# Kernel tuning notes

Measured on AMD Instinct MI355X. Metric: run time of the kernel, lower is better.

Reference implementation:

```python
import jax, jax.numpy as jnp
import numpy as np

B, C, S_TGT, S_MEM, D, NH, DK, DHID = 8, 1, 2048, 1024, 512, 2, 64, 1024
DQ4 = float(DK) ** 0.25  # dim_q ** (1/4) scaling used by LightAttention


def _light_mask(S, E):
    # torch: log(triu(ones(E, S)).T) -> (S, E); 0 where col <= row else -inf
    return jnp.where(jnp.arange(E)[None, :] <= jnp.arange(S)[:, None], 0.0, -jnp.inf)


def _mhla(x_q, x_kv, Wq, bq, Wk, bk, Wv, bv, Wo, bo, use_mask):
    # Wq/Wk/Wv: (h, d_in, 64); per-head linear projections done batched via einsum
    Q = jnp.einsum('bcsd,hde->hbcse', x_q, Wq) + bq[:, None, None, None, :]
    K = jnp.einsum('bcsd,hde->hbcse', x_kv, Wk) + bk[:, None, None, None, :]
    V = jnp.einsum('bcsd,hde->hbcse', x_kv, Wv) + bv[:, None, None, None, :]
    if use_mask:
        Q = Q + _light_mask(Q.shape[-2], Q.shape[-1])
    A = jax.nn.softmax(Q / DQ4, axis=-2)                      # row-softmax over seq
    Kt = jnp.swapaxes(K, -1, -2) / DQ4                        # (h,b,c,64,Skv)
    Bm = jnp.einsum('hbces,hbcsd->hbced', jax.nn.softmax(Kt, axis=-1), V)  # (h,b,c,64,64)
    Z = jnp.einsum('hbcqe,hbced->hbcqd', A, Bm)               # (h,b,c,Sq,64)
    h, b, c, sq, dk = Z.shape
    Zc = jnp.moveaxis(Z, 0, -2).reshape(b, c, sq, h * dk)     # head-major concat
    return Zc @ Wo + bo


def _ln(x, g, bta, eps=1e-5):
    # torch LayerNorm over the last 3 dims (C,H,dim), biased variance
    mu = x.mean(axis=(-3, -2, -1), keepdims=True)
    var = ((x - mu) ** 2).mean(axis=(-3, -2, -1), keepdims=True)
    return (x - mu) / jnp.sqrt(var + eps) * g + bta


def _lffn(x, E1, D1, E2, D2):
    h = (x @ E1) @ D1           # dim -> dim_bn -> dim_hid
    h = h * jax.nn.sigmoid(h)   # Swish; dropout is identity in eval
    return (h @ E2) @ D2        # dim_hid -> dim_bn -> dim


def setup_inputs() -> dict:
    key = jax.random.key(0)
    ks = jax.random.split(key, 32)
    n = lambda i, shape, fan: jax.random.normal(ks[i], shape, jnp.float32) / np.sqrt(fan)
    inp = {
        'mem': jax.random.normal(ks[0], (B, C, S_MEM, D), jnp.float32),
        'y': jax.random.normal(ks[1], (B, C, S_TGT, D), jnp.float32),
        # masked self-attention MHLA (2 heads)
        'Wq_sa': n(2, (NH, D, DK), D), 'bq_sa': jnp.zeros((NH, DK), jnp.float32),
        'Wk_sa': n(3, (NH, D, DK), D), 'bk_sa': jnp.zeros((NH, DK), jnp.float32),
        'Wv_sa': n(4, (NH, D, DK), D), 'bv_sa': jnp.zeros((NH, DK), jnp.float32),
        'Wo_sa': n(5, (NH * DK, D), NH * DK), 'bo_sa': jnp.zeros((D,), jnp.float32),
        # cross-attention MHLA (2 heads)
        'Wq_x': n(6, (NH, D, DK), D), 'bq_x': jnp.zeros((NH, DK), jnp.float32),
        'Wk_x': n(7, (NH, D, DK), D), 'bk_x': jnp.zeros((NH, DK), jnp.float32),
        'Wv_x': n(8, (NH, D, DK), D), 'bv_x': jnp.zeros((NH, DK), jnp.float32),
        'Wo_x': n(9, (NH * DK, D), NH * DK), 'bo_x': jnp.zeros((D,), jnp.float32),
        # LFFN (bias-free linears); dim_bn = S_TGT
        'E1': n(10, (D, S_TGT), D), 'D1': n(11, (S_TGT, DHID), S_TGT),
        'E2': n(12, (DHID, S_TGT), DHID), 'D2': n(13, (S_TGT, D), S_TGT),
        # LayerNorm affines over (C, H, dim)
        'g1': jnp.ones((C, S_TGT, D), jnp.float32), 'b1': jnp.zeros((C, S_TGT, D), jnp.float32),
        'g2': jnp.ones((C, S_TGT, D), jnp.float32), 'b2': jnp.zeros((C, S_TGT, D), jnp.float32),
        'g3': jnp.ones((C, S_TGT, D), jnp.float32), 'b3': jnp.zeros((C, S_TGT, D), jnp.float32),
    }
    return inp


def reference(mem, y, Wq_sa, bq_sa, Wk_sa, bk_sa, Wv_sa, bv_sa, Wo_sa, bo_sa,
              Wq_x, bq_x, Wk_x, bk_x, Wv_x, bv_x, Wo_x, bo_x,
              E1, D1, E2, D2, g1, b1, g2, b2, g3, b3):
    y = y + _mhla(y, y, Wq_sa, bq_sa, Wk_sa, bk_sa, Wv_sa, bv_sa, Wo_sa, bo_sa, True)
    y = _ln(y, g1, b1)
    y = y + _mhla(y, mem, Wq_x, bq_x, Wk_x, bk_x, Wv_x, bv_x, Wo_x, bo_x, False)
    y = _ln(y, g2, b2)
    y = y + _lffn(y, E1, D1, E2, D2)
    y = _ln(y, g3, b3)
    return y
```

## Files before the change

### kernel.cpp

```cpp
#include <hip/hip_runtime.h>
#include <hip/hip_bf16.h>

#define BB 8
#define STGT 2048
#define SMEM 1024
#define DD 512
#define NHH 2
#define DKK 64
#define DHIDN 1024
#define NCH 32

static constexpr float INV_DQ4 = 0.35355339059327373f;

typedef __bf16 bf16x8 __attribute__((ext_vector_type(8)));
typedef float f32x4 __attribute__((ext_vector_type(4)));
typedef __hip_bfloat16 bf16_t;

__device__ __forceinline__ float ldext(const void* p, size_t i, int gbf) {
    return gbf ? __bfloat162float(((const bf16_t*)p)[i]) : ((const float*)p)[i];
}

__device__ __forceinline__ float4 ldext4(const void* p, size_t i, int gbf) {
    float4 v;
    if (gbf) {
        ushort4 u = *(const ushort4*)((const bf16_t*)p + i);
        v.x = __bfloat162float(*(const bf16_t*)&u.x);
        v.y = __bfloat162float(*(const bf16_t*)&u.y);
        v.z = __bfloat162float(*(const bf16_t*)&u.z);
        v.w = __bfloat162float(*(const bf16_t*)&u.w);
    } else {
        v = *(const float4*)((const float*)p + i);
    }
    return v;
}

__device__ __forceinline__ ushort4 packbf4(float4 v) {
    ushort4 o;
    bf16_t b0 = __float2bfloat16(v.x), b1 = __float2bfloat16(v.y);
    bf16_t b2 = __float2bfloat16(v.z), b3 = __float2bfloat16(v.w);
    o.x = *(unsigned short*)&b0;
    o.y = *(unsigned short*)&b1;
    o.z = *(unsigned short*)&b2;
    o.w = *(unsigned short*)&b3;
    return o;
}

__device__ __forceinline__ void gld16(const bf16_t* g, bf16_t* l) {
    __builtin_amdgcn_global_load_lds(
        (const __attribute__((address_space(1))) unsigned int*)g,
        (__attribute__((address_space(3))) unsigned int*)l, 16, 0, 0);
}

__device__ __forceinline__ void sm_combine_block(const float* __restrict__ pstat, int mat,
                                                 float* smx, float* sinv, int t) {
    if (t < 64) {
        const int col = t;
        float m = -1e30f;
#pragma unroll 4
        for (int c2 = 0; c2 < NCH; ++c2)
            m = fmaxf(m, pstat[(size_t)(mat * NCH + c2) * 128 + col]);
        float s = 0.f;
#pragma unroll 4
        for (int c2 = 0; c2 < NCH; ++c2) {
            float pm = pstat[(size_t)(mat * NCH + c2) * 128 + col];
            float ps = pstat[(size_t)(mat * NCH + c2) * 128 + 64 + col];
            s += ps * __expf(pm - m);
        }
        smx[col] = m;
        sinv[col] = 1.f / s;
    }
}

__global__ void detect_k(const unsigned int* __restrict__ g1w, int* __restrict__ flag,
                         float* __restrict__ statp) {
    for (int i = threadIdx.x; i < 12288; i += 256) statp[i] = 0.f;
    if (threadIdx.x == 0) flag[0] = (g1w[0] == 0x3F800000u) ? 0 : 1;
}

__global__ __launch_bounds__(256) void gemm64_k(
    const bf16_t* __restrict__ A, int lda,
    const bf16_t* __restrict__ Bt, int ldb,
    void* C, int ldc, int obf,
    const float* __restrict__ bias,
    const void* Res, int ldr, int resbf,
    int K, int act, float* __restrict__ lnstats)
{
    __shared__ __align__(16) char smem[32768];
    bf16_t* sA = (bf16_t*)smem;
    bf16_t* sB = (bf16_t*)(smem + 16384);
    float* T = (float*)smem;

    const int t = threadIdx.x, lane = t & 63, wave = t >> 6;

    int bx = blockIdx.x, by = blockIdx.y;
    const int nbx = gridDim.x, nby = gridDim.y;
    if ((nby & 7) == 0) {
        int ord = by * nbx + bx;
        int grp = ord / (nbx * 8);
        int rem = ord - grp * nbx * 8;
        by = grp * 8 + (rem & 7);
        bx = rem >> 3;
    }
    const int m0 = by * 64, n0 = bx * 64;

    const int srow = t >> 3;
    const int schunk = ((t & 7) ^ (srow & 7)) * 8;
    const bf16_t* Ag = A + (size_t)(m0 + srow) * lda + schunk;
    const bf16_t* Ag1 = Ag + (size_t)32 * lda;
    const bf16_t* Bg = Bt + (size_t)(n0 + srow) * ldb + schunk;
    const bf16_t* Bg1 = Bg + (size_t)32 * ldb;
    const int wofs = t * 8;

    const int wm = wave >> 1, wn = wave & 1;
    const int fr = lane & 15, quad = lane >> 4;
    const int f7 = fr & 7;

    f32x4 acc[2][2];
#pragma unroll
    for (int i = 0; i < 2; ++i)
#pragma unroll
        for (int j = 0; j < 2; ++j) acc[i][j] = (f32x4){0.f, 0.f, 0.f, 0.f};

    gld16(Ag, sA + wofs);
    gld16(Ag1, sA + wofs + 2048);
    gld16(Bg, sB + wofs);
    gld16(Bg1, sB + wofs + 2048);

    int cur = 0;
    for (int k0 = 0; k0 < K; k0 += 64) {
        __builtin_amdgcn_s_waitcnt(0x0070);
        __builtin_amdgcn_s_barrier();
        if (k0 + 64 < K) {
            const int nxt = cur ^ 1;
            gld16(Ag + k0 + 64, sA + nxt * 4096 + wofs);
            gld16(Ag1 + k0 + 64, sA + nxt * 4096 + wofs + 2048);
            gld16(Bg + k0 + 64, sB + nxt * 4096 + wofs);
            gld16(Bg1 + k0 + 64, sB + nxt * 4096 + wofs + 2048);
        }
        const bf16_t* ab = sA + cur * 4096;
        const bf16_t* bb = sB + cur * 4096;
        bf16x8 af[2][2], bfv[2][2];
#pragma unroll
        for (int mf = 0; mf < 2; ++mf)
#pragma unroll
            for (int ks = 0; ks < 2; ++ks)
                af[mf][ks] = *(const bf16x8*)(ab + (wm * 32 + mf * 16 + fr) * 64 +
                                              (((ks * 4 + quad) ^ f7) * 8));
#pragma unroll
        for (int nf = 0; nf < 2; ++nf)
#pragma unroll
            for (int ks = 0; ks < 2; ++ks)
                bfv[nf][ks] = *(const bf16x8*)(bb + (wn * 32 + nf * 16 + fr) * 64 +
                                               (((ks * 4 + quad) ^ f7) * 8));
#pragma unroll
        for (int ks = 0; ks < 2; ++ks)
#pragma unroll
            for (int mf = 0; mf < 2; ++mf)
#pragma unroll
                for (int nf = 0; nf < 2; ++nf)
                    acc[mf][nf] = __builtin_amdgcn_mfma_f32_16x16x32_bf16(
                        af[mf][ks], bfv[nf][ks], acc[mf][nf], 0, 0, 0);
        cur ^= 1;
    }

    __syncthreads();
#pragma unroll
    for (int mf = 0; mf < 2; ++mf)
#pragma unroll
        for (int nf = 0; nf < 2; ++nf)
#pragma unroll
            for (int i = 0; i < 4; ++i)
                T[(wm * 32 + mf * 16 + quad * 4 + i) * 65 + wn * 32 + nf * 16 + fr] =
                    acc[mf][nf][i];
    __syncthreads();

    float s1 = 0.f, s2 = 0.f;
    const int tc4 = (t & 15) * 4;
    const int rb = t >> 4;
    float4 bv = {0.f, 0.f, 0.f, 0.f};
    if (bias) bv = *(const float4*)&bias[n0 + tc4];
#pragma unroll
    for (int rr = 0; rr < 4; ++rr) {
        const int row = rr * 16 + rb;
        const size_t grow = (size_t)(m0 + row);
        float4 v;
        v.x = T[row * 65 + tc4 + 0] + bv.x;
        v.y = T[row * 65 + tc4 + 1] + bv.y;
        v.z = T[row * 65 + tc4 + 2] + bv.z;
        v.w = T[row * 65 + tc4 + 3] + bv.w;
        if (act == 1) {
            v.x = v.x / (1.f + __expf(-v.x));
            v.y = v.y / (1.f + __expf(-v.y));
            v.z = v.z / (1.f + __expf(-v.z));
            v.w = v.w / (1.f + __expf(-v.w));
        }
        if (Res) {
            if (resbf) {
                ushort4 r = *(const ushort4*)((const bf16_t*)Res + grow * ldr + n0 + tc4);
                v.x += __bfloat162float(*(const bf16_t*)&r.x);
                v.y += __bfloat162float(*(const bf16_t*)&r.y);
                v.z += __bfloat162float(*(const bf16_t*)&r.z);
                v.w += __bfloat162float(*(const bf16_t*)&r.w);
            } else {
                float4 r = *(const float4*)((const float*)Res + grow * ldr + n0 + tc4);
                v.x += r.x;
                v.y += r.y;
                v.z += r.z;
                v.w += r.w;
            }
        }
        s1 += v.x + v.y + v.z + v.w;
        s2 += v.x * v.x + v.y * v.y + v.z * v.z + v.w * v.w;
        if (obf) {
            *(ushort4*)((bf16_t*)C + grow * ldc + n0 + tc4) = packbf4(v);
        } else {
            *(float4*)((float*)C + grow * ldc + n0 + tc4) = v;
        }
    }
    if (lnstats) {
        const int b2 = m0 >> 11;
#pragma unroll
        for (int o = 32; o > 0; o >>= 1) {
            s1 += __shfl_down(s1, o);
            s2 += __shfl_down(s2, o);
        }
        if (lane == 0) {
            const int bucket = ((bx * 7 + by) * 4 + wave) & 31;
            float* slot = &lnstats[(size_t)(b2 * 32 + bucket) * 16];
            atomicAdd(slot + 0, s1);
            atomicAdd(slot + 1, s2);
        }
    }
}

__global__ __launch_bounds__(256) void tr2_k(const void* __restrict__ D1s,
                                             const void* __restrict__ D2s,
                                             bf16_t* __restrict__ D1T,
                                             bf16_t* __restrict__ D2T,
                                             const int* __restrict__ gflag)
{
    const int z = blockIdx.z;
    if (z == 1 && blockIdx.x >= DD / 32) return;
    const void* S = z ? D2s : D1s;
    bf16_t* D = z ? D2T : D1T;
    const int ldS = z ? DD : DHIDN;
    const int ldD = STGT;
    const int gbf = *gflag;
    __shared__ float tile[32][33];
    const int c0 = blockIdx.x * 32, r0 = blockIdx.y * 32;
    const int tx = threadIdx.x, ty = threadIdx.y;
#pragma unroll
    for (int j = 0; j < 32; j += 8)
        tile[ty + j][tx] = ldext(S, (size_t)(r0 + ty + j) * ldS + c0 + tx, gbf);
    __syncthreads();
#pragma unroll
    for (int j = 0; j < 32; j += 8)
        D[(size_t)(c0 + ty + j) * ldD + r0 + tx] = __float2bfloat16(tile[tx][ty + j]);
}

__global__ __launch_bounds__(256) void tr8_k(
    const void* Wq_sa, const void* Wk_sa, const void* Wv_sa,
    const void* Wq_x, const void* Wk_x, const void* Wv_x,
    const void* Wo_sa, const void* Wo_x,
    const void* bq, const void* bk, const void* bv, const void* bqx, const void* bkx,
    const void* bvx, const void* bos, const void* box,
    bf16_t* __restrict__ WQKVT, bf16_t* __restrict__ WQXT, bf16_t* __restrict__ WKVXT,
    bf16_t* __restrict__ WOST, bf16_t* __restrict__ WOXT,
    float* __restrict__ biasd, const int* __restrict__ gflag)
{
    const int gbf = *gflag;
    const int blk = blockIdx.x;
    const int tx = threadIdx.x & 31, ty = threadIdx.x >> 5;

    if (blk >= 512) {
        const int i = (blk - 512) * 256 + threadIdx.x;
        if (i >= 1792) return;
        float v;
        if (i < 128) v = ldext(bq, i, gbf);
        else if (i < 256) v = ldext(bk, i - 128, gbf);
        else if (i < 384) v = ldext(bv, i - 256, gbf);
        else if (i < 512) v = ldext(bqx, i - 384, gbf);
        else if (i < 640) v = ldext(bkx, i - 512, gbf);
        else if (i < 768) v = ldext(bvx, i - 640, gbf);
        else if (i < 1280) v = ldext(bos, i - 768, gbf);
        else v = ldext(box, i - 1280, gbf);
        biasd[i] = v;
        return;
    }

    const void* src;
    bf16_t* dst;
    long soff;
    int ldS, ldD, c0, r0;
    if (blk < 384) {
        const int j = blk >> 5, m = j >> 1, h = j & 1, tid = blk & 31;
        c0 = (tid & 1) * 32;
        r0 = (tid >> 1) * 32;
        ldS = 64;
        ldD = 512;
        soff = (long)h * 32768;
        switch (m) {
            case 0: src = Wq_sa; dst = WQKVT + (0 + h * 64) * 512; break;
            case 1: src = Wk_sa; dst = WQKVT + (128 + h * 64) * 512; break;
            case 2: src = Wv_sa; dst = WQKVT + (256 + h * 64) * 512; break;
            case 3: src = Wq_x; dst = WQXT + h * 64 * 512; break;
            case 4: src = Wk_x; dst = WKVXT + h * 64 * 512; break;
            default: src = Wv_x; dst = WKVXT + (128 + h * 64) * 512; break;
        }
    } else {
        const int j = (blk - 384) >> 6, tid = (blk - 384) & 63;
        c0 = (tid & 15) * 32;
        r0 = (tid >> 4) * 32;
        ldS = 512;
        ldD = 128;
        soff = 0;
        src = j ? Wo_x : Wo_sa;
        dst = j ? WOXT : WOST;
    }

    __shared__ float tile[32][33];
#pragma unroll
    for (int j = 0; j < 32; j += 8)
        tile[ty + j][tx] = ldext(src, soff + (size_t)(r0 + ty + j) * ldS + c0 + tx, gbf);
    __syncthreads();
#pragma unroll
    for (int j = 0; j < 32; j += 8)
        dst[(size_t)(c0 + ty + j) * ldD + r0 + tx] = __float2bfloat16(tile[tx][ty + j]);
}

__global__ __launch_bounds__(256) void cvt_all_k(
    const void* __restrict__ Ys, const void* __restrict__ Ms,
    const void* __restrict__ E1s, const void* __restrict__ E2s,
    bf16_t* __restrict__ Yd, bf16_t* __restrict__ Md,
    bf16_t* __restrict__ E1d, bf16_t* __restrict__ E2d,
    const int* __restrict__ gflag)
{
    const int gbf = *gflag;
    const size_t gidx = (size_t)blockIdx.x * 256 + threadIdx.x;
    const void* src;
    bf16_t* dst;
    size_t off;
    if (gidx < 2097152) { src = Ys; dst = Yd; off = gidx * 4; }
    else if (gidx < 3145728) { src = Ms; dst = Md; off = (gidx - 2097152) * 4; }
    else if (gidx < 3407872) { src = E1s; dst = E1d; off = (gidx - 3145728) * 4; }
    else { src = E2s; dst = E2d; off = (gidx - 3407872) * 4; }
    if (gbf) {
        *(ushort4*)(dst + off) = *(const ushort4*)((const bf16_t*)src + off);
    } else {
        *(ushort4*)(dst + off) = packbf4(*(const float4*)((const float*)src + off));
    }
}

__global__ __launch_bounds__(256) void sm_partial2_k(
    const bf16_t* __restrict__ bufA, int ldA, int cofsA, int SA, int mA,
    const bf16_t* __restrict__ bufB, int ldB, int cofsB, int SB, int mB,
    float* __restrict__ pstat)
{
    const int z = blockIdx.z;
    const bf16_t* buf = z ? bufB : bufA;
    const int ld = z ? ldB : ldA, cofs = z ? cofsB : cofsA, S = z ? SB : SA,
              masked = z ? mB : mA;
    const int c = blockIdx.x, blk = blockIdx.y, mat = z * 16 + blk;
    const int h = blk / BB, b = blk % BB;
    const int rows = S / NCH, r0 = c * rows;
    const bf16_t* Mt = buf + (size_t)b * S * ld + cofs + h * 64;
    const int col = threadIdx.x & 63, rg = threadIdx.x >> 6;
    __shared__ float red[4][64];

    float mx = -1e30f;
    for (int r = r0 + rg; r < r0 + rows; r += 4)
        if (!masked || r >= col)
            mx = fmaxf(mx, __bfloat162float(Mt[(size_t)r * ld + col]) * INV_DQ4);
    red[rg][col] = mx;
    __syncthreads();
    mx = fmaxf(fmaxf(red[0][col], red[1][col]), fmaxf(red[2][col], red[3][col]));
    __syncthreads();

    float sm = 0.f;
    for (int r = r0 + rg; r < r0 + rows; r += 4)
        if (!masked || r >= col)
            sm += __expf(__bfloat162float(Mt[(size_t)r * ld + col]) * INV_DQ4 - mx);
    red[rg][col] = sm;
    __syncthreads();
    if (rg == 0) {
        sm = red[0][col] + red[1][col] + red[2][col] + red[3][col];
        pstat[(size_t)(mat * NCH + c) * 128 + col] = mx;
        pstat[(size_t)(mat * NCH + c) * 128 + 64 + col] = sm;
    }
}

__global__ __launch_bounds__(256) void bm_part_k(const bf16_t* __restrict__ buf, int ld,
                                                 int kofs, int vofs,
                                                 float* __restrict__ part, int S,
                                                 const float* __restrict__ pstat)
{
    const int c = blockIdx.x, blk = blockIdx.y;
    const int h = blk / BB, b = blk % BB;
    const bf16_t* Kp = buf + (size_t)b * S * ld + kofs + h * 64;
    const bf16_t* Vp = buf + (size_t)b * S * ld + vofs + h * 64;
    const int r0 = c * 128;
    __shared__ float sK[64][64];
    __shared__ float sV[64][64];
    __shared__ float smx[64], sinv[64];
    const int t = threadIdx.x;
    const int d = t & 63;
    const int eg = t >> 6;

    sm_combine_block(pstat, 16 + blk, smx, sinv, t);
    __syncthreads();

    float acc[16] = {};
    for (int s0 = r0; s0 < r0 + 128; s0 += 64) {
#pragma unroll
        for (int i = 0; i < 16; ++i) {
            int idx = i * 256 + t;
            int r = idx >> 6, cc = idx & 63;
            float kraw = __bfloat162float(Kp[(size_t)(s0 + r) * ld + cc]);
            sK[r][cc] = __expf(kraw * INV_DQ4 - smx[cc]) * sinv[cc];
            sV[r][cc] = __bfloat162float(Vp[(size_t)(s0 + r) * ld + cc]);
        }
        __syncthreads();
        for (int s = 0; s < 64; ++s) {
            float v = sV[s][d];
#pragma unroll
            for (int k = 0; k < 16; ++k) acc[k] += sK[s][eg * 16 + k] * v;
        }
        __syncthreads();
    }
    float* out = part + ((size_t)blk * gridDim.x + c) * 4096;
#pragma unroll
    for (int k = 0; k < 16; ++k) out[(size_t)(eg * 16 + k) * 64 + d] = acc[k];
}

__global__ __launch_bounds__(256) void bm_red_k(const float* __restrict__ part,
                                                float* __restrict__ Bm, int nch)
{
    const int i = blockIdx.x * 256 + threadIdx.x;
    const int mat = i >> 12, idx = i & 4095;
    float s = 0.f;
    for (int c = 0; c < nch; ++c) s += part[((size_t)mat * nch + c) * 4096 + idx];
    Bm[i] = s;
}

__global__ __launch_bounds__(256) void z_k(const bf16_t* __restrict__ Abuf, int lda_,
                                           const float* __restrict__ Bm,
                                           bf16_t* __restrict__ Zc, int S, int masked,
                                           const float* __restrict__ pstat)
{
    const int st = blockIdx.x, b = blockIdx.y, h = blockIdx.z;
    const int blk = h * BB + b;
    const bf16_t* Ap = Abuf + ((size_t)b * S + st * 64) * lda_ + h * 64;
    const float* Bp = Bm + (size_t)blk * 4096;
    __shared__ float sA[64][64];
    __shared__ float sBm[64][64];
    __shared__ float smx[64], sinv[64];
    const int t = threadIdx.x;
    const int d = t & 63;
    const int rg = t >> 6;

    sm_combine_block(pstat, blk, smx, sinv, t);
    __syncthreads();

#pragma unroll
    for (int i = 0; i < 16; ++i) {
        int idx = i * 256 + t;
        int r = idx >> 6, c = idx & 63;
        float qraw = __bfloat162float(Ap[(size_t)r * lda_ + c]);
        float v = 0.f;
        if (!masked || (st * 64 + r) >= c)
            v = __expf(qraw * INV_DQ4 - smx[c]) * sinv[c];
        sA[r][c] = v;
        sBm[r][c] = Bp[(size_t)r * 64 + c];
    }
    __syncthreads();
    float acc[16] = {};
    for (int e = 0; e < 64; ++e) {
        float bv = sBm[e][d];
#pragma unroll
        for (int k = 0; k < 16; ++k) acc[k] += sA[rg * 16 + k][e] * bv;
    }
    const int sbase = st * 64;
#pragma unroll
    for (int k = 0; k < 16; ++k) {
        int s = sbase + rg * 16 + k;
        Zc[((size_t)(b * STGT + s)) * 128 + h * 64 + d] = __float2bfloat16(acc[k]);
    }
}

__global__ __launch_bounds__(256) void ln_norm_k(const void* __restrict__ X, int inbf,
                                                 const float* __restrict__ statp,
                                                 const void* __restrict__ g,
                                                 const void* __restrict__ bt, void* Y,
                                                 int outmode, int per_b,
                                                 const int* __restrict__ gflag)
{
    __shared__ float sst[2];
    const int gbf = *gflag;
    const size_t i0 = ((size_t)blockIdx.x * 256 + threadIdx.x) * 4;
    const int b = (int)(((size_t)blockIdx.x * 1024) / per_b);
    const int t = threadIdx.x;
    if (t < 64) {
        const int j = t >> 5;
        const int k = t & 31;
        float v = statp[(size_t)(b * 32 + k) * 16 + j];
#pragma unroll
        for (int o = 16; o > 0; o >>= 1) v += __shfl_down(v, o, 32);
        if (k == 0) sst[j] = v;
    }
    __syncthreads();
    const size_t w = i0 % per_b;
    const float invn = 1.f / (float)per_b;
    float mu = sst[0] * invn;
    float var = sst[1] * invn - mu * mu;
    float inv = rsqrtf(fmaxf(var, 0.f) + 1e-5f);

    float4 xv = ldext4(X, i0, inbf);
    float4 gv = ldext4(g, w, gbf);
    float4 bv = ldext4(bt, w, gbf);
    float4 v;
    v.x = (xv.x - mu) * inv * gv.x + bv.x;
    v.y = (xv.y - mu) * inv * gv.y + bv.y;
    v.z = (xv.z - mu) * inv * gv.z + bv.z;
    v.w = (xv.w - mu) * inv * gv.w + bv.w;
    if (outmode == 0 || gbf) {
        *(ushort4*)((bf16_t*)Y + i0) = packbf4(v);
    } else {
        *(float4*)((float*)Y + i0) = v;
    }
}

static void gemm64x(hipStream_t s, const bf16_t* A, int lda, const bf16_t* Bt, int ldb,
                    void* C, int ldc, int obf, const float* bias, const void* Res, int ldr,
                    int resbf, int M, int N, int K, int act, float* lnstats)
{
    gemm64_k<<<dim3(N / 64, M / 64), 256, 0, s>>>(A, lda, Bt, ldb, C, ldc, obf, bias, Res, ldr,
                                                  resbf, K, act, lnstats);
}

static constexpr size_t OFF_XBF = 0;
static constexpr size_t OFF_YBF = 8388608;
static constexpr size_t OFF_REG = 12582912;
static constexpr size_t OFF_ZC = 18874368;
static constexpr size_t OFF_MEMBF = 19922944;
static constexpr size_t OFF_BM = 22020096;
static constexpr size_t OFF_W1T = 22085632;
static constexpr size_t OFF_W2T = 22347776;
static constexpr size_t OFF_WQKVT = 22609920;
static constexpr size_t OFF_WQXT = 22708224;
static constexpr size_t OFF_WKVXT = 22740992;
static constexpr size_t OFF_WOST = 22806528;
static constexpr size_t OFF_WOXT = 22839296;
static constexpr size_t OFF_BIAS = 22872064;
static constexpr size_t OFF_FLAG = 22874160;
static constexpr size_t OFF_PST = 22874176;
static constexpr size_t OFF_BMP = 23009344;
static constexpr size_t OFF_STP = 24057920;

extern "C" void kernel_launch(void* const* d_in, const int* in_sizes, int n_in,
                              void* d_out, int out_size, void* d_ws, size_t ws_size,
                              hipStream_t stream)
{
    const void* mem = d_in[0];
    const void* yin = d_in[1];
    const void* Wq_sa = d_in[2];
    const void* bq_sa = d_in[3];
    const void* Wk_sa = d_in[4];
    const void* bk_sa = d_in[5];
    const void* Wv_sa = d_in[6];
    const void* bv_sa = d_in[7];
    const void* Wo_sa = d_in[8];
    const void* bo_sa = d_in[9];
    const void* Wq_x = d_in[10];
    const void* bq_x = d_in[11];
    const void* Wk_x = d_in[12];
    const void* bk_x = d_in[13];
    const void* Wv_x = d_in[14];
    const void* bv_x = d_in[15];
    const void* Wo_x = d_in[16];
    const void* bo_x = d_in[17];
    const void* E1 = d_in[18];
    const void* D1 = d_in[19];
    const void* E2 = d_in[20];
    const void* D2 = d_in[21];
    const void* g1 = d_in[22];
    const void* b1 = d_in[23];
    const void* g2 = d_in[24];
    const void* b2 = d_in[25];
    const void* g3 = d_in[26];
    const void* b3 = d_in[27];

    float* ws = (float*)d_ws;
    bf16_t* xbf = (bf16_t*)(ws + OFF_XBF);
    bf16_t* ybf = (bf16_t*)(ws + OFF_YBF);
    float* REG = ws + OFF_REG;
    bf16_t* Zc = (bf16_t*)(ws + OFF_ZC);
    bf16_t* membf = (bf16_t*)(ws + OFF_MEMBF);
    float* Bmb = ws + OFF_BM;
    bf16_t* W1T = (bf16_t*)(ws + OFF_W1T);
    bf16_t* W2T = (bf16_t*)(ws + OFF_W2T);
    bf16_t* WQKVT = (bf16_t*)(ws + OFF_WQKVT);
    bf16_t* WQXT = (bf16_t*)(ws + OFF_WQXT);
    bf16_t* WKVXT = (bf16_t*)(ws + OFF_WKVXT);
    bf16_t* WOST = (bf16_t*)(ws + OFF_WOST);
    bf16_t* WOXT = (bf16_t*)(ws + OFF_WOXT);
    float* bias = ws + OFF_BIAS;
    int* gflag = (int*)(ws + OFF_FLAG);
    float* pstat = ws + OFF_PST;
    float* bmpart = ws + OFF_BMP;
    float* statp = ws + OFF_STP;

    bf16_t* E1bf = (bf16_t*)REG;
    bf16_t* D1T = (bf16_t*)REG + 1048576;
    bf16_t* E2bf = (bf16_t*)REG + 3145728;
    bf16_t* D2T = (bf16_t*)REG + 5242880;
    bf16_t* QKVs = (bf16_t*)REG;
    bf16_t* Qx = (bf16_t*)REG;
    bf16_t* KVx = (bf16_t*)REG + 2097152;
    bf16_t* hbuf = (bf16_t*)REG;

    const int MQ = BB * STGT;
    const int MK = BB * SMEM;
    const int per_b = STGT * DD;
    const int total = BB * per_b;
    const dim3 trb(32, 8);

    detect_k<<<1, 256, 0, stream>>>((const unsigned int*)g1, gflag, statp);

    cvt_all_k<<<15360, 256, 0, stream>>>(yin, mem, E1, E2, ybf, membf, E1bf, E2bf, gflag);

    tr2_k<<<dim3(DHIDN / 32, STGT / 32, 2), trb, 0, stream>>>(D1, D2, D1T, D2T, gflag);
    tr8_k<<<519, 256, 0, stream>>>(Wq_sa, Wk_sa, Wv_sa, Wq_x, Wk_x, Wv_x, Wo_sa, Wo_x,
                                   bq_sa, bk_sa, bv_sa, bq_x, bk_x, bv_x, bo_sa, bo_x,
                                   WQKVT, WQXT, WKVXT, WOST, WOXT, bias, gflag);

    gemm64x(stream, D1T, STGT, E1bf, STGT, W1T, DD, 1, nullptr, nullptr, 0, 0, DHIDN, DD,
            STGT, 0, nullptr);
    gemm64x(stream, D2T, STGT, E2bf, STGT, W2T, DHIDN, 1, nullptr, nullptr, 0, 0, DD, DHIDN,
            STGT, 0, nullptr);

    gemm64x(stream, ybf, DD, WQKVT, DD, QKVs, 384, 1, bias + 0, nullptr, 0, 0, MQ, 384, DD, 0,
            nullptr);
    sm_partial2_k<<<dim3(NCH, 16, 2), 256, 0, stream>>>(QKVs, 384, 0, STGT, 1, QKVs, 384, 128,
                                                        STGT, 0, pstat);
    bm_part_k<<<dim3(STGT / 128, 16), 256, 0, stream>>>(QKVs, 384, 128, 256, bmpart, STGT,
                                                        pstat);
    bm_red_k<<<(16 * 4096) / 256, 256, 0, stream>>>(bmpart, Bmb, STGT / 128);
    z_k<<<dim3(STGT / 64, BB, NHH), 256, 0, stream>>>(QKVs, 384, Bmb, Zc, STGT, 1, pstat);
    gemm64x(stream, Zc, 128, WOST, 128, xbf, DD, 1, bias + 768, ybf, DD, 1, MQ, DD, 128, 0,
            statp + 0);
    ln_norm_k<<<total / 1024, 256, 0, stream>>>(xbf, 1, statp + 0, g1, b1, ybf, 0, per_b,
                                                gflag);

    gemm64x(stream, ybf, DD, WQXT, DD, Qx, 128, 1, bias + 384, nullptr, 0, 0, MQ, 128, DD, 0,
            nullptr);
    gemm64x(stream, membf, DD, WKVXT, DD, KVx, 256, 1, bias + 512, nullptr, 0, 0, MK, 256, DD,
            0, nullptr);
    sm_partial2_k<<<dim3(NCH, 16, 2), 256, 0, stream>>>(Qx, 128, 0, STGT, 0, KVx, 256, 0, SMEM,
                                                        0, pstat);
    bm_part_k<<<dim3(SMEM / 128, 16), 256, 0, stream>>>(KVx, 256, 0, 128, bmpart, SMEM, pstat);
    bm_red_k<<<(16 * 4096) / 256, 256, 0, stream>>>(bmpart, Bmb, SMEM / 128);
    z_k<<<dim3(STGT / 64, BB, NHH), 256, 0, stream>>>(Qx, 128, Bmb, Zc, STGT, 0, pstat);
    gemm64x(stream, Zc, 128, WOXT, 128, xbf, DD, 1, bias + 1280, ybf, DD, 1, MQ, DD, 128, 0,
            statp + 4096);
    ln_norm_k<<<total / 1024, 256, 0, stream>>>(xbf, 1, statp + 4096, g2, b2, ybf, 0, per_b,
                                                gflag);

    gemm64x(stream, ybf, DD, W1T, DD, hbuf, DHIDN, 1, nullptr, nullptr, 0, 0, MQ, DHIDN, DD,
            1, nullptr);
    gemm64x(stream, hbuf, DHIDN, W2T, DHIDN, xbf, DD, 1, nullptr, ybf, DD, 1, MQ, DD, DHIDN,
            0, statp + 8192);

    ln_norm_k<<<total / 1024, 256, 0, stream>>>(xbf, 1, statp + 8192, g3, b3, d_out, 2, per_b,
                                                gflag);
}
```

Measured before the change: 502.9 us.

## Fuse softmax partial statistics into QKV projection GEMM epilogue

Computes per-64-row-tile column max and exp-sum of scaled Q/K directly in the GEMM epilogue and writes them to the partial-stat buffer, removing the separate sm_partial2_k passes. The combine step now takes the chunk count derived from sequence length. This avoids two kernel launches and a re-read of the projected Q/K tensors, at the cost of extra synchronisation and exp work in the GEMM epilogue.

```diff
diff --git a/kernel.cpp b/kernel.cpp
--- a/kernel.cpp
+++ b/kernel.cpp
@@ -45,6 +45,10 @@
     return o;
 }
 
+__device__ __forceinline__ float bfr(float v) {
+    return __bfloat162float(__float2bfloat16(v));
+}
+
 __device__ __forceinline__ void gld16(const bf16_t* g, bf16_t* l) {
     __builtin_amdgcn_global_load_lds(
         (const __attribute__((address_space(1))) unsigned int*)g,
@@ -52,16 +56,16 @@
 }
 
 __device__ __forceinline__ void sm_combine_block(const float* __restrict__ pstat, int mat,
-                                                 float* smx, float* sinv, int t) {
+                                                 float* smx, float* sinv, int t, int nch) {
     if (t < 64) {
         const int col = t;
         float m = -1e30f;
 #pragma unroll 4
-        for (int c2 = 0; c2 < NCH; ++c2)
+        for (int c2 = 0; c2 < nch; ++c2)
             m = fmaxf(m, pstat[(size_t)(mat * NCH + c2) * 128 + col]);
         float s = 0.f;
 #pragma unroll 4
-        for (int c2 = 0; c2 < NCH; ++c2) {
+        for (int c2 = 0; c2 < nch; ++c2) {
             float pm = pstat[(size_t)(mat * NCH + c2) * 128 + col];
             float ps = pstat[(size_t)(mat * NCH + c2) * 128 + 64 + col];
             s += ps * __expf(pm - m);
@@ -83,7 +87,8 @@
     void* C, int ldc, int obf,
     const float* __restrict__ bias,
     const void* Res, int ldr, int resbf,
-    int K, int act, float* __restrict__ lnstats)
+    int K, int act, float* __restrict__ lnstats,
+    float* __restrict__ pstat, int q_hi, int k_lo, int k_hi, int Srows, int selfmask)
 {
     __shared__ __align__(16) char smem[32768];
     bf16_t* sA = (bf16_t*)smem;
@@ -179,6 +184,7 @@
     const int rb = t >> 4;
     float4 bv = {0.f, 0.f, 0.f, 0.f};
     if (bias) bv = *(const float4*)&bias[n0 + tc4];
+    float4 vals[4];
 #pragma unroll
     for (int rr = 0; rr < 4; ++rr) {
         const int row = rr * 16 + rb;
@@ -216,7 +222,64 @@
         } else {
             *(float4*)((float*)C + grow * ldc + n0 + tc4) = v;
         }
-    }
+        vals[rr] = v;
+    }
+
+    if (pstat != nullptr) {
+        const int bidx = m0 / Srows;
+        const int chunk = (m0 % Srows) >> 6;
+        int mat = -1;
+        if (n0 < q_hi) mat = (n0 >> 6) * BB + bidx;
+        else if (n0 >= k_lo && n0 < k_hi) mat = 16 + ((n0 - k_lo) >> 6) * BB + bidx;
+        if (mat >= 0) {
+            const int qmask = selfmask && (n0 < q_hi) && ((m0 % Srows) == 0);
+            float* RM = (float*)smem;
+            float* RS = (float*)smem + 1024;
+            float* CMX = (float*)smem + 2048;
+            __syncthreads();
+            float lm[4] = {-1e30f, -1e30f, -1e30f, -1e30f};
+#pragma unroll
+            for (int rr = 0; rr < 4; ++rr) {
+                const int rt = rr * 16 + rb;
+                float fx[4] = {vals[rr].x, vals[rr].y, vals[rr].z, vals[rr].w};
+#pragma unroll
+                for (int j = 0; j < 4; ++j)
+                    if (!qmask || rt >= tc4 + j)
+                        lm[j] = fmaxf(lm[j], bfr(fx[j]) * INV_DQ4);
+            }
+#pragma unroll
+            for (int j = 0; j < 4; ++j) RM[rb * 64 + tc4 + j] = lm[j];
+            __syncthreads();
+            if (t < 64) {
+                float cm = -1e30f;
+#pragma unroll
+                for (int k2 = 0; k2 < 16; ++k2) cm = fmaxf(cm, RM[k2 * 64 + t]);
+                CMX[t] = cm;
+            }
+            __syncthreads();
+            float ls[4] = {0.f, 0.f, 0.f, 0.f};
+#pragma unroll
+            for (int rr = 0; rr < 4; ++rr) {
+                const int rt = rr * 16 + rb;
+                float fx[4] = {vals[rr].x, vals[rr].y, vals[rr].z, vals[rr].w};
+#pragma unroll
+                for (int j = 0; j < 4; ++j)
+                    if (!qmask || rt >= tc4 + j)
+                        ls[j] += __expf(bfr(fx[j]) * INV_DQ4 - CMX[tc4 + j]);
+            }
+#pragma unroll
+            for (int j = 0; j < 4; ++j) RS[rb * 64 + tc4 + j] = ls[j];
+            __syncthreads();
+            if (t < 64) {
+                float s = 0.f;
+#pragma unroll
+                for (int k2 = 0; k2 < 16; ++k2) s += RS[k2 * 64 + t];
+                pstat[((size_t)mat * NCH + chunk) * 128 + t] = CMX[t];
+                pstat[((size_t)mat * NCH + chunk) * 128 + 64 + t] = s;
+            }
+        }
+    }
+
     if (lnstats) {
         const int b2 = m0 >> 11;
 #pragma unroll
@@ -351,44 +414,6 @@
     }
 }
 
-__global__ __launch_bounds__(256) void sm_partial2_k(
-    const bf16_t* __restrict__ bufA, int ldA, int cofsA, int SA, int mA,
-    const bf16_t* __restrict__ bufB, int ldB, int cofsB, int SB, int mB,
-    float* __restrict__ pstat)
-{
-    const int z = blockIdx.z;
-    const bf16_t* buf = z ? bufB : bufA;
-    const int ld = z ? ldB : ldA, cofs = z ? cofsB : cofsA, S = z ? SB : SA,
-              masked = z ? mB : mA;
-    const int c = blockIdx.x, blk = blockIdx.y, mat = z * 16 + blk;
-    const int h = blk / BB, b = blk % BB;
-    const int rows = S / NCH, r0 = c * rows;
-    const bf16_t* Mt = buf + (size_t)b * S * ld + cofs + h * 64;
-    const int col = threadIdx.x & 63, rg = threadIdx.x >> 6;
-    __shared__ float red[4][64];
-
-    float mx = -1e30f;
-    for (int r = r0 + rg; r < r0 + rows; r += 4)
-        if (!masked || r >= col)
-            mx = fmaxf(mx, __bfloat162float(Mt[(size_t)r * ld + col]) * INV_DQ4);
-    red[rg][col] = mx;
-    __syncthreads();
-    mx = fmaxf(fmaxf(red[0][col], red[1][col]), fmaxf(red[2][col], red[3][col]));
-    __syncthreads();
-
-    float sm = 0.f;
-    for (int r = r0 + rg; r < r0 + rows; r += 4)
-        if (!masked || r >= col)
-            sm += __expf(__bfloat162float(Mt[(size_t)r * ld + col]) * INV_DQ4 - mx);
-    red[rg][col] = sm;
-    __syncthreads();
-    if (rg == 0) {
-        sm = red[0][col] + red[1][col] + red[2][col] + red[3][col];
-        pstat[(size_t)(mat * NCH + c) * 128 + col] = mx;
-        pstat[(size_t)(mat * NCH + c) * 128 + 64 + col] = sm;
-    }
-}
-
 __global__ __launch_bounds__(256) void bm_part_k(const bf16_t* __restrict__ buf, int ld,
                                                  int kofs, int vofs,
                                                  float* __restrict__ part, int S,
@@ -406,7 +431,7 @@
     const int d = t & 63;
     const int eg = t >> 6;
 
-    sm_combine_block(pstat, 16 + blk, smx, sinv, t);
+    sm_combine_block(pstat, 16 + blk, smx, sinv, t, S >> 6);
     __syncthreads();
 
     float acc[16] = {};
@@ -458,7 +483,7 @@
     const int d = t & 63;
     const int rg = t >> 6;
 
-    sm_combine_block(pstat, blk, smx, sinv, t);
+    sm_combine_block(pstat, blk, smx, sinv, t, S >> 6);
     __syncthreads();
 
 #pragma unroll
@@ -531,10 +556,13 @@
 
 static void gemm64x(hipStream_t s, const bf16_t* A, int lda, const bf16_t* Bt, int ldb,
                     void* C, int ldc, int obf, const float* bias, const void* Res, int ldr,
-                    int resbf, int M, int N, int K, int act, float* lnstats)
+                    int resbf, int M, int N, int K, int act, float* lnstats,
+                    float* pstat = nullptr, int q_hi = 0, int k_lo = 0, int k_hi = 0,
+                    int Srows = STGT, int selfmask = 0)
 {
     gemm64_k<<<dim3(N / 64, M / 64), 256, 0, s>>>(A, lda, Bt, ldb, C, ldc, obf, bias, Res, ldr,
-                                                  resbf, K, act, lnstats);
+                                                  resbf, K, act, lnstats, pstat, q_hi, k_lo,
+                                                  k_hi, Srows, selfmask);
 }
 
 static constexpr size_t OFF_XBF = 0;
@@ -639,9 +667,7 @@
             STGT, 0, nullptr);
 
     gemm64x(stream, ybf, DD, WQKVT, DD, QKVs, 384, 1, bias + 0, nullptr, 0, 0, MQ, 384, DD, 0,
-            nullptr);
-    sm_partial2_k<<<dim3(NCH, 16, 2), 256, 0, stream>>>(QKVs, 384, 0, STGT, 1, QKVs, 384, 128,
-                                                        STGT, 0, pstat);
+            nullptr, pstat, 128, 128, 256, STGT, 1);
     bm_part_k<<<dim3(STGT / 128, 16), 256, 0, stream>>>(QKVs, 384, 128, 256, bmpart, STGT,
                                                         pstat);
     bm_red_k<<<(16 * 4096) / 256, 256, 0, stream>>>(bmpart, Bmb, STGT / 128);
@@ -652,11 +678,9 @@
                                                 gflag);
 
     gemm64x(stream, ybf, DD, WQXT, DD, Qx, 128, 1, bias + 384, nullptr, 0, 0, MQ, 128, DD, 0,
-            nullptr);
+            nullptr, pstat, 128, 0, 0, STGT, 0);
     gemm64x(stream, membf, DD, WKVXT, DD, KVx, 256, 1, bias + 512, nullptr, 0, 0, MK, 256, DD,
-            0, nullptr);
-    sm_partial2_k<<<dim3(NCH, 16, 2), 256, 0, stream>>>(Qx, 128, 0, STGT, 0, KVx, 256, 0, SMEM,
-                                                        0, pstat);
+            0, nullptr, pstat, 0, 0, 128, SMEM, 0);
     bm_part_k<<<dim3(SMEM / 128, 16), 256, 0, stream>>>(KVx, 256, 0, 128, bmpart, SMEM, pstat);
     bm_red_k<<<(16 * 4096) / 256, 256, 0, stream>>>(bmpart, Bmb, SMEM / 128);
     z_k<<<dim3(STGT / 64, BB, NHH), 256, 0, stream>>>(Qx, 128, Bmb, Zc, STGT, 0, pstat);
```

Result: faster. 481.2 us (-4.3%).
